# Performance work log

Measured on AMD Instinct MI355X. Metric: run time of the kernel, lower is better.

Reference implementation:

```python
import jax, jax.numpy as jnp
import numpy as np

N_LIG, N_TGT, E = 100000, 4000, 150000
D_LIG, D_TGT, H = 4, 1280, 128


def _seg_mean(feat, idx, n):
    # segment mean; isolated nodes get 0 (PyG mean aggr semantics)
    s = jax.ops.segment_sum(feat, idx, num_segments=n)
    c = jax.ops.segment_sum(jnp.ones((idx.shape[0], 1), feat.dtype), idx, num_segments=n)
    return s / jnp.maximum(c, 1.0)


def setup_inputs() -> dict:
    key = jax.random.key(0)
    ks = jax.random.split(key, 20)
    s = 0.05  # weight scale
    inp = {
        'x_ligand': jax.random.normal(ks[0], (N_LIG, D_LIG), jnp.float32),
        'x_target': jax.random.normal(ks[1], (N_TGT, D_TGT), jnp.float32),
        'edge_index': jnp.stack([
            jax.random.randint(ks[2], (E,), 0, N_LIG, jnp.int32),
            jax.random.randint(ks[3], (E,), 0, N_TGT, jnp.int32),
        ]),
        'W1lt_l': jax.random.normal(ks[4], (D_LIG, H), jnp.float32) * s,
        'b1lt':   jax.random.normal(ks[5], (H,), jnp.float32) * s,
        'W1lt_r': jax.random.normal(ks[6], (D_TGT, H), jnp.float32) * s,
        'W1tl_l': jax.random.normal(ks[7], (D_TGT, H), jnp.float32) * s,
        'b1tl':   jax.random.normal(ks[8], (H,), jnp.float32) * s,
        'W1tl_r': jax.random.normal(ks[9], (D_LIG, H), jnp.float32) * s,
        'W2lt_l': jax.random.normal(ks[10], (H, H), jnp.float32) * s,
        'b2lt':   jax.random.normal(ks[11], (H,), jnp.float32) * s,
        'W2lt_r': jax.random.normal(ks[12], (H, H), jnp.float32) * s,
        'W2tl_l': jax.random.normal(ks[13], (H, H), jnp.float32) * s,
        'b2tl':   jax.random.normal(ks[14], (H,), jnp.float32) * s,
        'W2tl_r': jax.random.normal(ks[15], (H, H), jnp.float32) * s,
        'Wp':     jax.random.normal(ks[16], (2 * H, 1), jnp.float32) * s,
        'bp':     jax.random.normal(ks[17], (1,), jnp.float32) * s,
    }
    return inp


def reference(x_ligand, x_target, edge_index,
              W1lt_l, b1lt, W1lt_r, W1tl_l, b1tl, W1tl_r,
              W2lt_l, b2lt, W2lt_r, W2tl_l, b2tl, W2tl_r, Wp, bp):
    src, dst = edge_index[0], edge_index[1]  # ligand idx, target idx

    # conv1: SAGEConv  out = lin_l(mean_j x_src[j]) + lin_r(x_dst)
    m_t = _seg_mean(x_ligand[src], dst, N_TGT)              # [N_TGT, D_LIG]
    h_t = m_t @ W1lt_l + b1lt + x_target @ W1lt_r           # [N_TGT, H]
    m_l = _seg_mean(x_target[dst], src, N_LIG)              # [N_LIG, D_TGT]
    h_l = m_l @ W1tl_l + b1tl + x_ligand @ W1tl_r           # [N_LIG, H]
    h_t = jax.nn.relu(h_t)
    h_l = jax.nn.relu(h_l)

    # conv2 (hidden -> hidden), same edge structure
    m_t2 = _seg_mean(h_l[src], dst, N_TGT)
    h_t2 = jax.nn.relu(m_t2 @ W2lt_l + b2lt + h_t @ W2lt_r)
    m_l2 = _seg_mean(h_t[dst], src, N_LIG)
    h_l2 = jax.nn.relu(m_l2 @ W2tl_l + b2tl + h_l @ W2tl_r)

    # edge predictor: gather-cat-linear
    edge_feats = jnp.concatenate([h_l2[src], h_t2[dst]], axis=-1)  # [E, 2H]
    out = (edge_feats @ Wp + bp).squeeze(-1)                        # [E]
    return out
```

## Files before the change

### kernel.cpp

```cpp
#include <hip/hip_runtime.h>
#include <hip/hip_bf16.h>

#define N_LIG 100000
#define N_TGT 4000
#define NEDGE 150000
#define DT 1280
#define HD 128
#define CAP_L 32
#define CAP_T 128
#define NTILE_L 6250
#define NTILE_PAD 6252
#define PL_BLOCKS 1563

typedef __attribute__((ext_vector_type(8))) short short8v;
typedef __attribute__((ext_vector_type(4))) float f32x4;

static __device__ __forceinline__ ushort f2bf(float f) {
    __hip_bfloat16 h = __float2bfloat16(f);
    union { __hip_bfloat16 h; ushort u; } c; c.h = h; return c.u;
}
static __device__ __forceinline__ float bf2f(ushort u) {
    union { unsigned v; float f; } c; c.v = ((unsigned)u) << 16; return c.f;
}

__global__ __launch_bounds__(256) void k_pack(
    const float* __restrict__ W2, uint4* __restrict__ Wf,
    const float* __restrict__ Wr, const float* __restrict__ Wl,
    uint4* __restrict__ Wf1,
    const float* __restrict__ xt, uint4* __restrict__ xtf,
    int4* __restrict__ cntz,
    const float* __restrict__ W2a, const float* __restrict__ W2b,
    uint4* __restrict__ Wf2)
{
    int bx = blockIdx.x;
    if (bx < 8) {
        int gid = bx * 256 + threadIdx.x;
        int lane = gid & 63, frag = gid >> 6;
        int ks = frag >> 3, ct = frag & 7;
        int l15 = lane & 15, g = lane >> 4;
        int k = ks * 32 + g * 4, n = ct * 16 + l15;
        union { ushort us[8]; uint4 u; } o;
#pragma unroll
        for (int j = 0; j < 4; ++j) {
            o.us[j]     = f2bf(W2[(size_t)(k + j) * HD + n]);
            o.us[4 + j] = f2bf(W2[(size_t)(k + 16 + j) * HD + n]);
        }
        Wf[gid] = o.u;
    } else if (bx < 168) {
        int gid = (bx - 8) * 256 + threadIdx.x;
        int lane = gid & 63, frag = gid >> 6;
        int ks = frag >> 4, nct = frag & 15;
        int l15 = lane & 15, g = lane >> 4;
        int k = ks * 32 + g * 4, n = nct * 16 + l15;
        const float* Ws = (n < HD) ? Wr : Wl;
        int nn = n & 127;
        union { ushort us[8]; uint4 u; } o;
#pragma unroll
        for (int j = 0; j < 4; ++j) {
            o.us[j]     = f2bf(Ws[(size_t)(k + j) * HD + nn]);
            o.us[4 + j] = f2bf(Ws[(size_t)(k + 16 + j) * HD + nn]);
        }
        Wf1[gid] = o.u;
    } else if (bx < 2668) {
        int gid = (bx - 168) * 256 + threadIdx.x;
        int lane = gid & 63, frag = gid >> 6;
        int ks = frag % 40, rt = frag / 40;
        int row = rt * 16 + (lane & 15);
        int kb = ks * 32 + (lane >> 4) * 4;
        float4 a0 = *reinterpret_cast<const float4*>(xt + (size_t)row * DT + kb);
        float4 a1 = *reinterpret_cast<const float4*>(xt + (size_t)row * DT + kb + 16);
        union { ushort us[8]; uint4 u; } o;
        o.us[0] = f2bf(a0.x); o.us[1] = f2bf(a0.y); o.us[2] = f2bf(a0.z); o.us[3] = f2bf(a0.w);
        o.us[4] = f2bf(a1.x); o.us[5] = f2bf(a1.y); o.us[6] = f2bf(a1.z); o.us[7] = f2bf(a1.w);
        xtf[gid] = o.u;
    } else if (bx < 2770) {
        int i = (bx - 2668) * 256 + threadIdx.x;
        if (i < 26000) cntz[i] = make_int4(0, 0, 0, 0);
    } else {
        int gid = (bx - 2770) * 256 + threadIdx.x;
        int lane = gid & 63, frag = gid >> 6;
        int ks = frag >> 4, nct = frag & 15;
        int l15 = lane & 15, g = lane >> 4;
        int k = ks * 32 + g * 4, n = nct * 16 + l15;
        const float* Ws = (n < HD) ? W2a : W2b;
        int nn = n & 127;
        union { ushort us[8]; uint4 u; } o;
#pragma unroll
        for (int j = 0; j < 4; ++j) {
            o.us[j]     = f2bf(Ws[(size_t)(k + j) * HD + nn]);
            o.us[4 + j] = f2bf(Ws[(size_t)(k + 16 + j) * HD + nn]);
        }
        Wf2[gid] = o.u;
    }
}

__global__ __launch_bounds__(256) void k_fill(
    const int* __restrict__ src, const int* __restrict__ dst,
    int* __restrict__ cnt_src, int* __restrict__ cnt_dst,
    int* __restrict__ bsrc, int* __restrict__ bdst)
{
    int e = blockIdx.x * 256 + threadIdx.x;
    if (e >= NEDGE) return;
    int s = src[e], d = dst[e];
    int ps = atomicAdd(&cnt_src[s], 1);
    if (ps < CAP_L) bsrc[(size_t)s * CAP_L + ps] = d;
    int pd = atomicAdd(&cnt_dst[d], 1);
    if (pd < CAP_T) bdst[(size_t)d * CAP_T + pd] = s;
}

__global__ __launch_bounds__(512) void k_tgt1m(
    const uint4* __restrict__ xtf,
    const uint4* __restrict__ Wf1,
    const uint4* __restrict__ Wf2,
    const float* __restrict__ xl,
    const int* __restrict__ bdst, const int* __restrict__ cnt_dst,
    const float* __restrict__ W1lt_l,
    const float* __restrict__ b1lt,
    float* __restrict__ y_t1,
    float* __restrict__ y_t2, float* __restrict__ htW2r)
{
    __shared__ float  ms[16][4];
    __shared__ ushort hts[16][136];

    int w = threadIdx.x >> 6;
    int lane = threadIdx.x & 63;
    int l15 = lane & 15, g = lane >> 4;
    int rt = blockIdx.x;
    int row0 = rt * 16;

    if (threadIdx.x < 128) {
        int r = threadIdx.x >> 3, lane8 = threadIdx.x & 7;
        int row = row0 + r;
        int deg = cnt_dst[row];
        int n = min(deg, CAP_T);
        float4 acc = make_float4(0.f, 0.f, 0.f, 0.f);
        for (int i = lane8; i < n; i += 8) {
            int sid = bdst[(size_t)row * CAP_T + i];
            float4 x = *reinterpret_cast<const float4*>(xl + 4ull * (unsigned)sid);
            acc.x += x.x; acc.y += x.y; acc.z += x.z; acc.w += x.w;
        }
#pragma unroll
        for (int off = 1; off < 8; off <<= 1) {
            acc.x += __shfl_xor(acc.x, off); acc.y += __shfl_xor(acc.y, off);
            acc.z += __shfl_xor(acc.z, off); acc.w += __shfl_xor(acc.w, off);
        }
        if (lane8 == 0) {
            float dinv = 1.0f / fmaxf((float)deg, 1.0f);
            ms[r][0] = acc.x * dinv; ms[r][1] = acc.y * dinv;
            ms[r][2] = acc.z * dinv; ms[r][3] = acc.w * dinv;
        }
    }

    f32x4 acc[2];
#pragma unroll
    for (int ct = 0; ct < 2; ++ct) acc[ct] = (f32x4){0.f, 0.f, 0.f, 0.f};

    for (int ks = 0; ks < DT / 32; ++ks) {
        union { uint4 u; short8v s; } ua;
        ua.u = xtf[(size_t)(rt * 40 + ks) * 64 + lane];
#pragma unroll
        for (int ct = 0; ct < 2; ++ct) {
            union { uint4 u; short8v s; } ub;
            ub.u = Wf1[(size_t)(ks * 16 + w * 2 + ct) * 64 + lane];
            acc[ct] = __builtin_amdgcn_mfma_f32_16x16x32_bf16(ua.s, ub.s, acc[ct], 0, 0, 0);
        }
    }

    __syncthreads();

    if (w < 4) {
#pragma unroll
        for (int ct = 0; ct < 2; ++ct) {
            int c = w * 32 + ct * 16 + l15;
            float wl0 = W1lt_l[c], wl1 = W1lt_l[HD + c],
                  wl2 = W1lt_l[2 * HD + c], wl3 = W1lt_l[3 * HD + c];
            float bb = b1lt[c];
#pragma unroll
            for (int j = 0; j < 4; ++j) {
                int r = 4 * g + j;
                float v = acc[ct][j] + bb + ms[r][0] * wl0 + ms[r][1] * wl1
                        + ms[r][2] * wl2 + ms[r][3] * wl3;
                hts[r][c] = f2bf(fmaxf(v, 0.0f));
            }
        }
    } else {
#pragma unroll
        for (int ct = 0; ct < 2; ++ct) {
            int c = (w - 4) * 32 + ct * 16 + l15;
#pragma unroll
            for (int j = 0; j < 4; ++j) {
                int grow = row0 + 4 * g + j;
                y_t1[(size_t)grow * HD + c] = acc[ct][j];
            }
        }
    }
    __syncthreads();

    f32x4 acc2[2];
#pragma unroll
    for (int ct = 0; ct < 2; ++ct) acc2[ct] = (f32x4){0.f, 0.f, 0.f, 0.f};

#pragma unroll
    for (int ks2 = 0; ks2 < 4; ++ks2) {
        int kb2 = ks2 * 32 + g * 4;
        union { ushort us[8]; short8v s; } ua2;
        *reinterpret_cast<ushort4*>(&ua2.us[0]) =
            *reinterpret_cast<const ushort4*>(&hts[l15][kb2]);
        *reinterpret_cast<ushort4*>(&ua2.us[4]) =
            *reinterpret_cast<const ushort4*>(&hts[l15][kb2 + 16]);
#pragma unroll
        for (int ct = 0; ct < 2; ++ct) {
            union { uint4 u; short8v s; } ub2;
            ub2.u = Wf2[(size_t)(ks2 * 16 + w * 2 + ct) * 64 + lane];
            acc2[ct] = __builtin_amdgcn_mfma_f32_16x16x32_bf16(ua2.s, ub2.s, acc2[ct], 0, 0, 0);
        }
    }

    float* outp = (w < 4) ? y_t2 : htW2r;
    int cw = (w < 4) ? w : (w - 4);
#pragma unroll
    for (int ct = 0; ct < 2; ++ct) {
        int c = cw * 32 + ct * 16 + l15;
#pragma unroll
        for (int j = 0; j < 4; ++j) {
            int grow = row0 + 4 * g + j;
            outp[(size_t)grow * HD + c] = acc2[ct][j];
        }
    }
}

__global__ __launch_bounds__(256) void k_hl(
    const float* __restrict__ xl, const float* __restrict__ y_t1,
    const int* __restrict__ bsrc, const int* __restrict__ cnt_src,
    const float* __restrict__ W1tl_r,
    const float* __restrict__ b1tl,
    ushort* __restrict__ hlb, uint4* __restrict__ hlbf)
{
    int tc = threadIdx.x & 15;
    int node = blockIdx.x * 16 + (threadIdx.x >> 4);
    int ks = tc >> 2, g = tc & 3;
    int kb = ks * 32 + g * 4;

    int deg = cnt_src[node];
    int n = min(deg, CAP_L);
    float4 s0 = make_float4(0.f, 0.f, 0.f, 0.f);
    float4 s1 = make_float4(0.f, 0.f, 0.f, 0.f);
    for (int i = 0; i < n; ++i) {
        int did = bsrc[(size_t)node * CAP_L + i];
        float4 v0 = *reinterpret_cast<const float4*>(y_t1 + (size_t)did * HD + kb);
        float4 v1 = *reinterpret_cast<const float4*>(y_t1 + (size_t)did * HD + kb + 16);
        s0.x += v0.x; s0.y += v0.y; s0.z += v0.z; s0.w += v0.w;
        s1.x += v1.x; s1.y += v1.y; s1.z += v1.z; s1.w += v1.w;
    }
    float dinv = 1.0f / fmaxf((float)deg, 1.0f);
    float4 x = *reinterpret_cast<const float4*>(xl + 4ull * (unsigned)node);

    float4 b0 = *reinterpret_cast<const float4*>(b1tl + kb);
    float4 b1 = *reinterpret_cast<const float4*>(b1tl + kb + 16);
    float4 wa0 = *reinterpret_cast<const float4*>(W1tl_r + 0 * HD + kb);
    float4 wa1 = *reinterpret_cast<const float4*>(W1tl_r + 1 * HD + kb);
    float4 wa2 = *reinterpret_cast<const float4*>(W1tl_r + 2 * HD + kb);
    float4 wa3 = *reinterpret_cast<const float4*>(W1tl_r + 3 * HD + kb);
    float4 wb0 = *reinterpret_cast<const float4*>(W1tl_r + 0 * HD + kb + 16);
    float4 wb1 = *reinterpret_cast<const float4*>(W1tl_r + 1 * HD + kb + 16);
    float4 wb2 = *reinterpret_cast<const float4*>(W1tl_r + 2 * HD + kb + 16);
    float4 wb3 = *reinterpret_cast<const float4*>(W1tl_r + 3 * HD + kb + 16);

    union { ushort us[8]; uint4 u; ushort4 h[2]; } o;
    o.us[0] = f2bf(fmaxf(s0.x * dinv + b0.x + x.x * wa0.x + x.y * wa1.x + x.z * wa2.x + x.w * wa3.x, 0.f));
    o.us[1] = f2bf(fmaxf(s0.y * dinv + b0.y + x.x * wa0.y + x.y * wa1.y + x.z * wa2.y + x.w * wa3.y, 0.f));
    o.us[2] = f2bf(fmaxf(s0.z * dinv + b0.z + x.x * wa0.z + x.y * wa1.z + x.z * wa2.z + x.w * wa3.z, 0.f));
    o.us[3] = f2bf(fmaxf(s0.w * dinv + b0.w + x.x * wa0.w + x.y * wa1.w + x.z * wa2.w + x.w * wa3.w, 0.f));
    o.us[4] = f2bf(fmaxf(s1.x * dinv + b1.x + x.x * wb0.x + x.y * wb1.x + x.z * wb2.x + x.w * wb3.x, 0.f));
    o.us[5] = f2bf(fmaxf(s1.y * dinv + b1.y + x.x * wb0.y + x.y * wb1.y + x.z * wb2.y + x.w * wb3.y, 0.f));
    o.us[6] = f2bf(fmaxf(s1.z * dinv + b1.z + x.x * wb0.z + x.y * wb1.z + x.z * wb2.z + x.w * wb3.z, 0.f));
    o.us[7] = f2bf(fmaxf(s1.w * dinv + b1.w + x.x * wb0.w + x.y * wb1.w + x.z * wb2.w + x.w * wb3.w, 0.f));

    *reinterpret_cast<ushort4*>(hlb + (size_t)node * HD + kb)      = o.h[0];
    *reinterpret_cast<ushort4*>(hlb + (size_t)node * HD + kb + 16) = o.h[1];
    int lane = (node & 15) + 16 * g;
    hlbf[(size_t)(blockIdx.x * 4 + ks) * 64 + lane] = o.u;
}

__global__ __launch_bounds__(256) void k_ptl(
    const ushort* __restrict__ hlb,
    const uint4* __restrict__ hlbf,
    const uint4* __restrict__ Wf,
    const float* __restrict__ y_t2,
    const int* __restrict__ bsrc, const int* __restrict__ cnt_src,
    const int* __restrict__ bdst, const int* __restrict__ cnt_dst,
    const float* __restrict__ Wlt,
    const float* __restrict__ b2lt,
    const float* __restrict__ b2tl,
    const float* __restrict__ htW2r,
    const float* __restrict__ Wp,
    float* __restrict__ p_t, float* __restrict__ p_l)
{
    __shared__ int   idx[CAP_T];
    __shared__ float sm[16][132];
    __shared__ float msh[HD];
    __shared__ float sum2[2];

    if (blockIdx.x < N_TGT) {
        int row = blockIdx.x;
        int deg = cnt_dst[row];
        int nn = min(deg, CAP_T);

        if (threadIdx.x < CAP_T) idx[threadIdx.x] = bdst[(size_t)row * CAP_T + threadIdx.x];
        __syncthreads();

        int wg = threadIdx.x >> 4, l16 = threadIdx.x & 15;
        float s[8];
#pragma unroll
        for (int j = 0; j < 8; ++j) s[j] = 0.f;
        for (int i = wg; i < nn; i += 16) {
            int sid = idx[i];
            union { uint4 u; ushort us[8]; } v;
            v.u = *reinterpret_cast<const uint4*>(hlb + (size_t)sid * HD + l16 * 8);
#pragma unroll
            for (int j = 0; j < 8; ++j) s[j] += bf2f(v.us[j]);
        }
#pragma unroll
        for (int j = 0; j < 8; ++j) sm[wg][l16 * 8 + j] = s[j];
        __syncthreads();

        if (threadIdx.x < HD) {
            int h = threadIdx.x;
            float dinv = 1.0f / fmaxf((float)deg, 1.0f);
            float acc = 0.f;
#pragma unroll
            for (int w2 = 0; w2 < 16; ++w2) acc += sm[w2][h];
            msh[h] = acc * dinv;
        }
        __syncthreads();

        if (threadIdx.x < HD) {
            int h = threadIdx.x;
            float g = 0.f;
            for (int k = 0; k < HD; k += 4) {
                float4 mk = *reinterpret_cast<const float4*>(&msh[k]);
                g += mk.x * Wlt[(size_t)(k + 0) * HD + h] + mk.y * Wlt[(size_t)(k + 1) * HD + h]
                   + mk.z * Wlt[(size_t)(k + 2) * HD + h] + mk.w * Wlt[(size_t)(k + 3) * HD + h];
            }
            float v = fmaxf(g + b2lt[h] + htW2r[(size_t)row * HD + h], 0.0f);
            float part = v * Wp[HD + h];
#pragma unroll
            for (int off = 1; off < 64; off <<= 1) part += __shfl_xor(part, off);
            if ((h & 63) == 0) sum2[h >> 6] = part;
        }
        __syncthreads();
        if (threadIdx.x == 0) p_t[row] = sum2[0] + sum2[1];
        return;
    }

    int wid = threadIdx.x >> 6;
    int lane = threadIdx.x & 63;
    int l15 = lane & 15, g = lane >> 4;
    int tile = (blockIdx.x - N_TGT) * 4 + wid;
    int wrow0 = tile * 16;

    f32x4 acc[8];
#pragma unroll
    for (int ct = 0; ct < 8; ++ct) acc[ct] = (f32x4){0.f, 0.f, 0.f, 0.f};

#pragma unroll
    for (int ks = 0; ks < 4; ++ks) {
        union { uint4 u; short8v s; } ua;
        ua.u = hlbf[(size_t)(tile * 4 + ks) * 64 + lane];
#pragma unroll
        for (int ct = 0; ct < 8; ++ct) {
            union { uint4 u; short8v s; } ub;
            ub.u = Wf[(ks * 8 + ct) * 64 + lane];
            acc[ct] = __builtin_amdgcn_mfma_f32_16x16x32_bf16(ua.s, ub.s, acc[ct], 0, 0, 0);
        }
    }

    float wpv[8], bv[8];
#pragma unroll
    for (int ct = 0; ct < 8; ++ct) {
        int c = ct * 16 + l15;
        wpv[ct] = Wp[c];
        bv[ct]  = b2tl[c];
    }

#pragma unroll
    for (int j = 0; j < 4; ++j) {
        int row = wrow0 + g * 4 + j;
        bool valid = row < N_LIG;
        int deg = valid ? cnt_src[row] : 0;
        int nn = min(deg, CAP_L);
        float dinv = 1.0f / fmaxf((float)deg, 1.0f);
        float s[8];
#pragma unroll
        for (int ct = 0; ct < 8; ++ct) s[ct] = 0.f;
        for (int i = 0; i < nn; ++i) {
            int did = bsrc[(size_t)row * CAP_L + i];
            const float* yp = y_t2 + (size_t)did * HD + l15;
#pragma unroll
            for (int ct = 0; ct < 8; ++ct) s[ct] += yp[ct * 16];
        }
        float part = 0.f;
#pragma unroll
        for (int ct = 0; ct < 8; ++ct) {
            float v = acc[ct][j] + s[ct] * dinv + bv[ct];
            part += fmaxf(v, 0.f) * wpv[ct];
        }
#pragma unroll
        for (int off = 1; off < 16; off <<= 1) part += __shfl_xor(part, off);
        if (valid && l15 == 0) p_l[row] = part;
    }
}

__global__ __launch_bounds__(256) void k_out(
    const int* __restrict__ src, const int* __restrict__ dst,
    const float* __restrict__ p_l, const float* __restrict__ p_t,
    const float* __restrict__ bp, float* __restrict__ out)
{
    int e = blockIdx.x * 256 + threadIdx.x;
    if (e >= NEDGE) return;
    out[e] = p_l[src[e]] + p_t[dst[e]] + bp[0];
}

extern "C" void kernel_launch(void* const* d_in, const int* in_sizes, int n_in,
                              void* d_out, int out_size, void* d_ws, size_t ws_size,
                              hipStream_t stream)
{
    const float* x_l    = (const float*)d_in[0];
    const float* x_t    = (const float*)d_in[1];
    const int*   ei     = (const int*)  d_in[2];
    const float* W1lt_l = (const float*)d_in[3];
    const float* b1lt   = (const float*)d_in[4];
    const float* W1lt_r = (const float*)d_in[5];
    const float* W1tl_l = (const float*)d_in[6];
    const float* b1tl   = (const float*)d_in[7];
    const float* W1tl_r = (const float*)d_in[8];
    const float* W2lt_l = (const float*)d_in[9];
    const float* b2lt   = (const float*)d_in[10];
    const float* W2lt_r = (const float*)d_in[11];
    const float* W2tl_l = (const float*)d_in[12];
    const float* b2tl   = (const float*)d_in[13];
    const float* W2tl_r = (const float*)d_in[14];
    const float* Wp     = (const float*)d_in[15];
    const float* bp     = (const float*)d_in[16];

    const int* src = ei;
    const int* dst = ei + NEDGE;

    char* ws = (char*)d_ws;
    size_t o = 0;
    int* cnt_src = (int*)(ws + o); o += (size_t)N_LIG * 4;
    int* cnt_dst = (int*)(ws + o); o += (size_t)N_TGT * 4;
    int* bsrc = (int*)(ws + o); o += (size_t)N_LIG * CAP_L * 4;
    int* bdst = (int*)(ws + o); o += (size_t)N_TGT * CAP_T * 4;
    ushort* hlb  = (ushort*)(ws + o); o += (size_t)N_LIG * HD * 2;
    uint4* hlbf  = (uint4*)(ws + o);  o += (size_t)NTILE_PAD * 4 * 64 * 16;
    uint4* Wf    = (uint4*)(ws + o);  o += (size_t)32 * 64 * 16;
    uint4* Wf1   = (uint4*)(ws + o);  o += (size_t)640 * 64 * 16;
    uint4* Wf2   = (uint4*)(ws + o);  o += (size_t)64 * 64 * 16;
    uint4* xtf   = (uint4*)(ws + o);  o += (size_t)10000 * 64 * 16;
    float* y_t1  = (float*)(ws + o); o += (size_t)N_TGT * HD * 4;
    float* y_t2  = (float*)(ws + o); o += (size_t)N_TGT * HD * 4;
    float* htW2r = (float*)(ws + o); o += (size_t)N_TGT * HD * 4;
    float* p_l   = (float*)(ws + o); o += (size_t)N_LIG * 4;
    float* p_t   = (float*)(ws + o); o += (size_t)N_TGT * 4;

    float* out = (float*)d_out;

    k_pack<<<2786, 256, 0, stream>>>(W2tl_r, Wf, W1lt_r, W1tl_l, Wf1,
                                     x_t, xtf, (int4*)cnt_src,
                                     W2tl_l, W2lt_r, Wf2);

    k_fill<<<(NEDGE + 255) / 256, 256, 0, stream>>>(src, dst, cnt_src, cnt_dst, bsrc, bdst);

    k_tgt1m<<<N_TGT / 16, 512, 0, stream>>>(xtf, Wf1, Wf2, x_l, bdst, cnt_dst,
                                            W1lt_l, b1lt, y_t1, y_t2, htW2r);

    k_hl<<<NTILE_L, 256, 0, stream>>>(x_l, y_t1, bsrc, cnt_src, W1tl_r, b1tl, hlb, hlbf);

    k_ptl<<<N_TGT + PL_BLOCKS, 256, 0, stream>>>(hlb, hlbf, Wf, y_t2,
                                                 bsrc, cnt_src, bdst, cnt_dst,
                                                 W2lt_l, b2lt, b2tl, htW2r, Wp,
                                                 p_t, p_l);

    k_out<<<(NEDGE + 255) / 256, 256, 0, stream>>>(src, dst, p_l, p_t, bp, out);
}
```

Measured before the change: 118.0 us.

## Scatter ligand hidden rows into per-target edge buffers instead of gathering

Edge fill now records, for each ligand edge, the slot position in the target's adjacency list. The ligand hidden-state kernel writes each bf16 row directly into a per-target contiguous edge buffer (push/scatter), so the target aggregation in k_ptl reads contiguous memory instead of gathering random ligand rows through an index list. This drops the hlb array and the index staging, but adds a larger edge buffer, an extra slot array, and repeated writes per edge, with a permuted column mapping in the reduction.

```diff
diff --git a/kernel.cpp b/kernel.cpp
--- a/kernel.cpp
+++ b/kernel.cpp
@@ -97,15 +97,18 @@
 __global__ __launch_bounds__(256) void k_fill(
     const int* __restrict__ src, const int* __restrict__ dst,
     int* __restrict__ cnt_src, int* __restrict__ cnt_dst,
-    int* __restrict__ bsrc, int* __restrict__ bdst)
+    int* __restrict__ bsrc, int* __restrict__ bdst, int* __restrict__ bslot)
 {
     int e = blockIdx.x * 256 + threadIdx.x;
     if (e >= NEDGE) return;
     int s = src[e], d = dst[e];
-    int ps = atomicAdd(&cnt_src[s], 1);
-    if (ps < CAP_L) bsrc[(size_t)s * CAP_L + ps] = d;
     int pd = atomicAdd(&cnt_dst[d], 1);
     if (pd < CAP_T) bdst[(size_t)d * CAP_T + pd] = s;
+    int ps = atomicAdd(&cnt_src[s], 1);
+    if (ps < CAP_L) {
+        bsrc[(size_t)s * CAP_L + ps] = d;
+        bslot[(size_t)s * CAP_L + ps] = (pd < CAP_T) ? (d * CAP_T + pd) : -1;
+    }
 }
 
 __global__ __launch_bounds__(512) void k_tgt1m(
@@ -232,9 +235,10 @@
 __global__ __launch_bounds__(256) void k_hl(
     const float* __restrict__ xl, const float* __restrict__ y_t1,
     const int* __restrict__ bsrc, const int* __restrict__ cnt_src,
+    const int* __restrict__ bslot,
     const float* __restrict__ W1tl_r,
     const float* __restrict__ b1tl,
-    ushort* __restrict__ hlb, uint4* __restrict__ hlbf)
+    uint4* __restrict__ hlbf, uint4* __restrict__ ebuf)
 {
     int tc = threadIdx.x & 15;
     int node = blockIdx.x * 16 + (threadIdx.x >> 4);
@@ -266,7 +270,7 @@
     float4 wb2 = *reinterpret_cast<const float4*>(W1tl_r + 2 * HD + kb + 16);
     float4 wb3 = *reinterpret_cast<const float4*>(W1tl_r + 3 * HD + kb + 16);
 
-    union { ushort us[8]; uint4 u; ushort4 h[2]; } o;
+    union { ushort us[8]; uint4 u; } o;
     o.us[0] = f2bf(fmaxf(s0.x * dinv + b0.x + x.x * wa0.x + x.y * wa1.x + x.z * wa2.x + x.w * wa3.x, 0.f));
     o.us[1] = f2bf(fmaxf(s0.y * dinv + b0.y + x.x * wa0.y + x.y * wa1.y + x.z * wa2.y + x.w * wa3.y, 0.f));
     o.us[2] = f2bf(fmaxf(s0.z * dinv + b0.z + x.x * wa0.z + x.y * wa1.z + x.z * wa2.z + x.w * wa3.z, 0.f));
@@ -276,19 +280,22 @@
     o.us[6] = f2bf(fmaxf(s1.z * dinv + b1.z + x.x * wb0.z + x.y * wb1.z + x.z * wb2.z + x.w * wb3.z, 0.f));
     o.us[7] = f2bf(fmaxf(s1.w * dinv + b1.w + x.x * wb0.w + x.y * wb1.w + x.z * wb2.w + x.w * wb3.w, 0.f));
 
-    *reinterpret_cast<ushort4*>(hlb + (size_t)node * HD + kb)      = o.h[0];
-    *reinterpret_cast<ushort4*>(hlb + (size_t)node * HD + kb + 16) = o.h[1];
     int lane = (node & 15) + 16 * g;
     hlbf[(size_t)(blockIdx.x * 4 + ks) * 64 + lane] = o.u;
+
+    for (int i = 0; i < n; ++i) {
+        int slot = bslot[(size_t)node * CAP_L + i];
+        if (slot >= 0) ebuf[(size_t)slot * 16 + tc] = o.u;
+    }
 }
 
 __global__ __launch_bounds__(256) void k_ptl(
-    const ushort* __restrict__ hlb,
+    const uint4* __restrict__ ebuf,
     const uint4* __restrict__ hlbf,
     const uint4* __restrict__ Wf,
     const float* __restrict__ y_t2,
     const int* __restrict__ bsrc, const int* __restrict__ cnt_src,
-    const int* __restrict__ bdst, const int* __restrict__ cnt_dst,
+    const int* __restrict__ cnt_dst,
     const float* __restrict__ Wlt,
     const float* __restrict__ b2lt,
     const float* __restrict__ b2tl,
@@ -296,7 +303,6 @@
     const float* __restrict__ Wp,
     float* __restrict__ p_t, float* __restrict__ p_l)
 {
-    __shared__ int   idx[CAP_T];
     __shared__ float sm[16][132];
     __shared__ float msh[HD];
     __shared__ float sum2[2];
@@ -306,17 +312,14 @@
         int deg = cnt_dst[row];
         int nn = min(deg, CAP_T);
 
-        if (threadIdx.x < CAP_T) idx[threadIdx.x] = bdst[(size_t)row * CAP_T + threadIdx.x];
-        __syncthreads();
-
         int wg = threadIdx.x >> 4, l16 = threadIdx.x & 15;
+        const uint4* base = ebuf + (size_t)row * CAP_T * 16;
         float s[8];
 #pragma unroll
         for (int j = 0; j < 8; ++j) s[j] = 0.f;
         for (int i = wg; i < nn; i += 16) {
-            int sid = idx[i];
             union { uint4 u; ushort us[8]; } v;
-            v.u = *reinterpret_cast<const uint4*>(hlb + (size_t)sid * HD + l16 * 8);
+            v.u = base[(size_t)i * 16 + l16];
 #pragma unroll
             for (int j = 0; j < 8; ++j) s[j] += bf2f(v.us[j]);
         }
@@ -326,11 +329,14 @@
 
         if (threadIdx.x < HD) {
             int h = threadIdx.x;
-            float dinv = 1.0f / fmaxf((float)deg, 1.0f);
+            int tc2 = h >> 3, jj = h & 7;
+            int idx2 = tc2 * 8 + jj;
             float acc = 0.f;
 #pragma unroll
-            for (int w2 = 0; w2 < 16; ++w2) acc += sm[w2][h];
-            msh[h] = acc * dinv;
+            for (int w2 = 0; w2 < 16; ++w2) acc += sm[w2][idx2];
+            int ks2 = tc2 >> 2, g2 = tc2 & 3;
+            int col = ks2 * 32 + ((jj >> 2) << 4) + g2 * 4 + (jj & 3);
+            msh[col] = acc / fmaxf((float)deg, 1.0f);
         }
         __syncthreads();
 
@@ -450,10 +456,11 @@
     size_t o = 0;
     int* cnt_src = (int*)(ws + o); o += (size_t)N_LIG * 4;
     int* cnt_dst = (int*)(ws + o); o += (size_t)N_TGT * 4;
-    int* bsrc = (int*)(ws + o); o += (size_t)N_LIG * CAP_L * 4;
-    int* bdst = (int*)(ws + o); o += (size_t)N_TGT * CAP_T * 4;
-    ushort* hlb  = (ushort*)(ws + o); o += (size_t)N_LIG * HD * 2;
+    int* bsrc  = (int*)(ws + o); o += (size_t)N_LIG * CAP_L * 4;
+    int* bslot = (int*)(ws + o); o += (size_t)N_LIG * CAP_L * 4;
+    int* bdst  = (int*)(ws + o); o += (size_t)N_TGT * CAP_T * 4;
     uint4* hlbf  = (uint4*)(ws + o);  o += (size_t)NTILE_PAD * 4 * 64 * 16;
+    uint4* ebuf  = (uint4*)(ws + o);  o += (size_t)N_TGT * CAP_T * 16 * 16;
     uint4* Wf    = (uint4*)(ws + o);  o += (size_t)32 * 64 * 16;
     uint4* Wf1   = (uint4*)(ws + o);  o += (size_t)640 * 64 * 16;
     uint4* Wf2   = (uint4*)(ws + o);  o += (size_t)64 * 64 * 16;
@@ -470,15 +477,17 @@
                                      x_t, xtf, (int4*)cnt_src,
                                      W2tl_l, W2lt_r, Wf2);
 
-    k_fill<<<(NEDGE + 255) / 256, 256, 0, stream>>>(src, dst, cnt_src, cnt_dst, bsrc, bdst);
+    k_fill<<<(NEDGE + 255) / 256, 256, 0, stream>>>(src, dst, cnt_src, cnt_dst,
+                                                    bsrc, bdst, bslot);
 
     k_tgt1m<<<N_TGT / 16, 512, 0, stream>>>(xtf, Wf1, Wf2, x_l, bdst, cnt_dst,
                                             W1lt_l, b1lt, y_t1, y_t2, htW2r);
 
-    k_hl<<<NTILE_L, 256, 0, stream>>>(x_l, y_t1, bsrc, cnt_src, W1tl_r, b1tl, hlb, hlbf);
-
-    k_ptl<<<N_TGT + PL_BLOCKS, 256, 0, stream>>>(hlb, hlbf, Wf, y_t2,
-                                                 bsrc, cnt_src, bdst, cnt_dst,
+    k_hl<<<NTILE_L, 256, 0, stream>>>(x_l, y_t1, bsrc, cnt_src, bslot,
+                                      W1tl_r, b1tl, hlbf, ebuf);
+
+    k_ptl<<<N_TGT + PL_BLOCKS, 256, 0, stream>>>(ebuf, hlbf, Wf, y_t2,
+                                                 bsrc, cnt_src, cnt_dst,
                                                  W2lt_l, b2lt, b2tl, htW2r, Wp,
                                                  p_t, p_l);
 
```

Result: slower. 121.6 us (+3.1%).

## Fuse second-layer ligand neighbor aggregation into the k_hl gather pass

Applied to the files above, without the earlier changes.

The mean over neighbouring targets of y_t2 (the second-layer target-to-ligand message) is now computed in k_hl, reusing the same neighbour index loop that already gathers y_t1. The result is stored as a bf16 buffer that k_ptl reads directly, so k_ptl no longer runs its own scalar gather loop per ligand row. This removes a second pass over bsrc and a set of poorly coalesced scalar loads. In exchange it writes and reads an extra 25.6MB bf16 buffer and rounds the aggregated term to bf16, which costs some precision.

```diff
diff --git a/kernel.cpp b/kernel.cpp
--- a/kernel.cpp
+++ b/kernel.cpp
@@ -230,11 +230,13 @@
 }
 
 __global__ __launch_bounds__(256) void k_hl(
-    const float* __restrict__ xl, const float* __restrict__ y_t1,
+    const float* __restrict__ xl,
+    const float* __restrict__ y_t1, const float* __restrict__ y_t2,
     const int* __restrict__ bsrc, const int* __restrict__ cnt_src,
     const float* __restrict__ W1tl_r,
     const float* __restrict__ b1tl,
-    ushort* __restrict__ hlb, uint4* __restrict__ hlbf)
+    ushort* __restrict__ hlb, uint4* __restrict__ hlbf,
+    ushort* __restrict__ gl2)
 {
     int tc = threadIdx.x & 15;
     int node = blockIdx.x * 16 + (threadIdx.x >> 4);
@@ -245,12 +247,18 @@
     int n = min(deg, CAP_L);
     float4 s0 = make_float4(0.f, 0.f, 0.f, 0.f);
     float4 s1 = make_float4(0.f, 0.f, 0.f, 0.f);
+    float4 t0 = make_float4(0.f, 0.f, 0.f, 0.f);
+    float4 t1 = make_float4(0.f, 0.f, 0.f, 0.f);
     for (int i = 0; i < n; ++i) {
         int did = bsrc[(size_t)node * CAP_L + i];
         float4 v0 = *reinterpret_cast<const float4*>(y_t1 + (size_t)did * HD + kb);
         float4 v1 = *reinterpret_cast<const float4*>(y_t1 + (size_t)did * HD + kb + 16);
+        float4 u0 = *reinterpret_cast<const float4*>(y_t2 + (size_t)did * HD + kb);
+        float4 u1 = *reinterpret_cast<const float4*>(y_t2 + (size_t)did * HD + kb + 16);
         s0.x += v0.x; s0.y += v0.y; s0.z += v0.z; s0.w += v0.w;
         s1.x += v1.x; s1.y += v1.y; s1.z += v1.z; s1.w += v1.w;
+        t0.x += u0.x; t0.y += u0.y; t0.z += u0.z; t0.w += u0.w;
+        t1.x += u1.x; t1.y += u1.y; t1.z += u1.z; t1.w += u1.w;
     }
     float dinv = 1.0f / fmaxf((float)deg, 1.0f);
     float4 x = *reinterpret_cast<const float4*>(xl + 4ull * (unsigned)node);
@@ -280,14 +288,21 @@
     *reinterpret_cast<ushort4*>(hlb + (size_t)node * HD + kb + 16) = o.h[1];
     int lane = (node & 15) + 16 * g;
     hlbf[(size_t)(blockIdx.x * 4 + ks) * 64 + lane] = o.u;
+
+    ushort4 q0, q1;
+    q0.x = f2bf(t0.x * dinv); q0.y = f2bf(t0.y * dinv);
+    q0.z = f2bf(t0.z * dinv); q0.w = f2bf(t0.w * dinv);
+    q1.x = f2bf(t1.x * dinv); q1.y = f2bf(t1.y * dinv);
+    q1.z = f2bf(t1.z * dinv); q1.w = f2bf(t1.w * dinv);
+    *reinterpret_cast<ushort4*>(gl2 + (size_t)node * HD + kb)      = q0;
+    *reinterpret_cast<ushort4*>(gl2 + (size_t)node * HD + kb + 16) = q1;
 }
 
 __global__ __launch_bounds__(256) void k_ptl(
     const ushort* __restrict__ hlb,
     const uint4* __restrict__ hlbf,
     const uint4* __restrict__ Wf,
-    const float* __restrict__ y_t2,
-    const int* __restrict__ bsrc, const int* __restrict__ cnt_src,
+    const ushort* __restrict__ gl2,
     const int* __restrict__ bdst, const int* __restrict__ cnt_dst,
     const float* __restrict__ Wlt,
     const float* __restrict__ b2lt,
@@ -387,22 +402,12 @@
     for (int j = 0; j < 4; ++j) {
         int row = wrow0 + g * 4 + j;
         bool valid = row < N_LIG;
-        int deg = valid ? cnt_src[row] : 0;
-        int nn = min(deg, CAP_L);
-        float dinv = 1.0f / fmaxf((float)deg, 1.0f);
-        float s[8];
-#pragma unroll
-        for (int ct = 0; ct < 8; ++ct) s[ct] = 0.f;
-        for (int i = 0; i < nn; ++i) {
-            int did = bsrc[(size_t)row * CAP_L + i];
-            const float* yp = y_t2 + (size_t)did * HD + l15;
-#pragma unroll
-            for (int ct = 0; ct < 8; ++ct) s[ct] += yp[ct * 16];
-        }
+        int lrow = valid ? row : 0;
+        const ushort* gp = gl2 + (size_t)lrow * HD + l15;
         float part = 0.f;
 #pragma unroll
         for (int ct = 0; ct < 8; ++ct) {
-            float v = acc[ct][j] + s[ct] * dinv + bv[ct];
+            float v = acc[ct][j] + bf2f(gp[ct * 16]) + bv[ct];
             part += fmaxf(v, 0.f) * wpv[ct];
         }
 #pragma unroll
@@ -453,6 +458,7 @@
     int* bsrc = (int*)(ws + o); o += (size_t)N_LIG * CAP_L * 4;
     int* bdst = (int*)(ws + o); o += (size_t)N_TGT * CAP_T * 4;
     ushort* hlb  = (ushort*)(ws + o); o += (size_t)N_LIG * HD * 2;
+    ushort* gl2  = (ushort*)(ws + o); o += (size_t)N_LIG * HD * 2;
     uint4* hlbf  = (uint4*)(ws + o);  o += (size_t)NTILE_PAD * 4 * 64 * 16;
     uint4* Wf    = (uint4*)(ws + o);  o += (size_t)32 * 64 * 16;
     uint4* Wf1   = (uint4*)(ws + o);  o += (size_t)640 * 64 * 16;
@@ -475,10 +481,11 @@
     k_tgt1m<<<N_TGT / 16, 512, 0, stream>>>(xtf, Wf1, Wf2, x_l, bdst, cnt_dst,
                                             W1lt_l, b1lt, y_t1, y_t2, htW2r);
 
-    k_hl<<<NTILE_L, 256, 0, stream>>>(x_l, y_t1, bsrc, cnt_src, W1tl_r, b1tl, hlb, hlbf);
-
-    k_ptl<<<N_TGT + PL_BLOCKS, 256, 0, stream>>>(hlb, hlbf, Wf, y_t2,
-                                                 bsrc, cnt_src, bdst, cnt_dst,
+    k_hl<<<NTILE_L, 256, 0, stream>>>(x_l, y_t1, y_t2, bsrc, cnt_src,
+                                      W1tl_r, b1tl, hlb, hlbf, gl2);
+
+    k_ptl<<<N_TGT + PL_BLOCKS, 256, 0, stream>>>(hlb, hlbf, Wf, gl2,
+                                                 bdst, cnt_dst,
                                                  W2lt_l, b2lt, b2tl, htW2r, Wp,
                                                  p_t, p_l);
 
```

After: 111.4 us, median of 2. 1.06x faster.
